# Kernel tuning notes

Hardware: AMD Instinct MI355X
Metric: run time of the kernel (lower is better)

## Reference

```python
import jax, jax.numpy as jnp
import numpy as np

B, L, E = 8, 2048, 128


def setup_inputs() -> dict:
    key = jax.random.key(0)
    k1, k2, k3, k4 = jax.random.split(key, 4)
    return {
        "Uq": jax.random.normal(k1, (B, L, E), dtype=jnp.float32),
        "Uid": jax.random.normal(k2, (B, L, E), dtype=jnp.float32),
        "mask": jnp.ones((L, L), dtype=jnp.float32),
        "Wc_w": jax.random.normal(k3, (3 * E,), dtype=jnp.float32) * 0.05,
        "Wc_b": jax.random.normal(k4, (), dtype=jnp.float32) * 0.05,
    }


def reference(Uq, Uid, mask, Wc_w, Wc_b):
    # Wc(cat(Uid, Uq, Uid*Uq)) decomposed into three direct projections —
    # exact same math as the Linear over the concatenation, never
    # materializing the [B, L, L, 3E] tensor.
    e = Uq.shape[-1]
    w_id, w_q, w_mul = Wc_w[:e], Wc_w[e:2 * e], Wc_w[2 * e:]
    s_id = jnp.einsum("bie,e->bi", Uid, w_id)          # [B, Lid]
    s_q = jnp.einsum("bje,e->bj", Uq, w_q)             # [B, Lq]
    s_mul = jnp.einsum("bie,bje,e->bij", Uid, Uq, w_mul)  # [B, Lid, Lq]
    S = (s_id[:, :, None] + s_q[:, None, :] + s_mul + Wc_b) * mask
    # S_D2Q = Softmax(dim=0) over the per-example [Lid, Lq] matrix -> axis=1
    P = jax.nn.softmax(S, axis=1)                      # [B, Lid, Lq]
    A_D2Q = jnp.einsum("bij,bje->bie", P, Uq)          # [B, Lid, E]
    M = jnp.einsum("bij,bkj->bik", P, P)               # P @ P^T, [B, Lid, Lid]
    A_Q2D = jnp.einsum("bik,bke->bie", M, Uid)         # [B, Lid, E]
    Vid = jnp.concatenate([Uid, A_D2Q, Uid * A_D2Q, Uid * A_Q2D], axis=-1)
    return Vid  # [B, Lid, 4E]
```

## Files before the change

### kernel.cpp

```cpp
#include <hip/hip_runtime.h>

#define L 2048
#define E 128
#define NB 8

typedef float f32x4 __attribute__((ext_vector_type(4)));
typedef short short8 __attribute__((ext_vector_type(8)));
typedef unsigned int u32;

static __device__ inline float bf2f(ushort u) {
  union { float f; u32 i; } v; v.i = ((u32)u) << 16; return v.f;
}
static __device__ inline ushort f2bf(float f) {
  union { float f; u32 i; } v; v.f = f;
  u32 x = v.i;
  return (ushort)((x + 0x7fffu + ((x >> 16) & 1u)) >> 16);
}

__device__ inline void glds16(const ushort* g, ushort* l) {
  __builtin_amdgcn_global_load_lds(
      (const __attribute__((address_space(1))) u32*)(const void*)g,
      (__attribute__((address_space(3))) u32*)(void*)l, 16, 0, 0);
}

__global__ __launch_bounds__(128) void k_prep(const float* __restrict__ Uq,
                                              const float* __restrict__ Uid,
                                              const float* __restrict__ Wcw,
                                              ushort* __restrict__ UqB,
                                              ushort* __restrict__ UidB,
                                              ushort* __restrict__ Uidw,
                                              float* __restrict__ s_id,
                                              float* __restrict__ s_q) {
  int r = blockIdx.x;
  int e = threadIdx.x;
  ushort uqu  = f2bf(Uq[(long)r * E + e]);
  ushort uidu = f2bf(Uid[(long)r * E + e]);
  float uqf = bf2f(uqu), uidf = bf2f(uidu);
  float wid  = bf2f(f2bf(Wcw[e]));
  float wq   = bf2f(f2bf(Wcw[E + e]));
  float wmul = bf2f(f2bf(Wcw[2 * E + e]));
  UqB[(long)r * E + e]  = uqu;
  UidB[(long)r * E + e] = uidu;
  Uidw[(long)r * E + e] = f2bf(uidf * wmul);
  float sid = uidf * wid, sq = uqf * wq;
  #pragma unroll
  for (int off = 32; off >= 1; off >>= 1) {
    sid += __shfl_down(sid, off, 64);
    sq  += __shfl_down(sq,  off, 64);
  }
  __shared__ float red[4];
  int wv = threadIdx.x >> 6;
  if ((threadIdx.x & 63) == 0) { red[wv * 2] = sid; red[wv * 2 + 1] = sq; }
  __syncthreads();
  if (threadIdx.x == 0) { s_id[r] = red[0] + red[2]; s_q[r] = red[1] + red[3]; }
}

__global__ __launch_bounds__(256) void k_maskT(const float* __restrict__ mask,
                                               ushort* __restrict__ maskT) {
  __shared__ ushort tile[32][33];
  int j0 = blockIdx.x * 32, i0 = blockIdx.y * 32;
  int tx = threadIdx.x, ty = threadIdx.y;
  #pragma unroll
  for (int r = ty; r < 32; r += 8)
    tile[r][tx] = f2bf(mask[(long)(i0 + r) * L + j0 + tx]);
  __syncthreads();
  #pragma unroll
  for (int r = ty; r < 32; r += 8)
    maskT[(long)(j0 + r) * L + i0 + tx] = tile[tx][r];
}

__global__ __launch_bounds__(256) void k_tr2(const ushort* __restrict__ s1,
                                             ushort* __restrict__ d1,
                                             const ushort* __restrict__ s2,
                                             ushort* __restrict__ d2) {
  __shared__ ushort tile[32][33];
  int zz = blockIdx.z;
  long base = (long)(zz & (NB - 1)) * L * E;
  const ushort* src = ((zz < NB) ? s1 : s2) + base;
  ushort* dst = ((zz < NB) ? d1 : d2) + base;
  int c0 = blockIdx.x * 32, r0 = blockIdx.y * 32;
  int tx = threadIdx.x, ty = threadIdx.y;
  #pragma unroll
  for (int i = ty; i < 32; i += 8)
    tile[i][tx] = src[(long)(r0 + i) * E + c0 + tx];
  __syncthreads();
  #pragma unroll
  for (int i = ty; i < 32; i += 8)
    dst[(long)(c0 + i) * L + r0 + tx] = tile[tx][i];
}

__device__ inline void gemm128_loop(const ushort* __restrict__ A,
                                    const ushort* __restrict__ B,
                                    long ldA, long ldB, int K,
                                    f32x4 acc[4][4],
                                    ushort* ldsA, ushort* ldsB) {
  const int t = threadIdx.x;
  const int w = t >> 6, lane = t & 63;
  const int mrow = lane & 15, quad = lane >> 4;
  const int lr = lane >> 3;
  const int lc = ((lane & 7) ^ lr) * 8;
  const int mh = (w & 1) * 64, nh = (w >> 1) * 64;
  for (int k0 = 0; k0 < K; k0 += 64) {
    __syncthreads();
    #pragma unroll
    for (int s = 0; s < 4; s++) {
      int row = w * 32 + s * 8 + lr;
      glds16(&A[(long)row * ldA + k0 + lc], &ldsA[w * 2048 + s * 512]);
      glds16(&B[(long)row * ldB + k0 + lc], &ldsB[w * 2048 + s * 512]);
    }
    __syncthreads();
    #pragma unroll
    for (int kk = 0; kk < 2; kk++) {
      short8 av[4], bv[4];
      #pragma unroll
      for (int mi = 0; mi < 4; mi++)
        av[mi] = *(const short8*)&ldsA[(mh + mi * 16 + mrow) * 64 +
                                       ((kk * 32 + quad * 8) ^ ((mrow & 7) << 3))];
      #pragma unroll
      for (int ni = 0; ni < 4; ni++)
        bv[ni] = *(const short8*)&ldsB[(nh + ni * 16 + mrow) * 64 +
                                       ((kk * 32 + quad * 8) ^ ((mrow & 7) << 3))];
      #pragma unroll
      for (int mi = 0; mi < 4; mi++)
        #pragma unroll
        for (int ni = 0; ni < 4; ni++)
          acc[mi][ni] = __builtin_amdgcn_mfma_f32_16x16x32_bf16(av[mi], bv[ni], acc[mi][ni], 0, 0, 0);
    }
  }
}

__device__ inline void gemm64x128_loop(const ushort* __restrict__ A,
                                       const ushort* __restrict__ B,
                                       long ldA, long ldB, int K,
                                       f32x4 acc[2][4],
                                       ushort* ldsA, ushort* ldsB) {
  const int t = threadIdx.x;
  const int w = t >> 6, lane = t & 63;
  const int mrow = lane & 15, quad = lane >> 4;
  const int lr = lane >> 3;
  const int lc = ((lane & 7) ^ lr) * 8;
  const int mh = (w & 1) * 32, nh = (w >> 1) * 64;
  for (int k0 = 0; k0 < K; k0 += 64) {
    __syncthreads();
    #pragma unroll
    for (int s = 0; s < 2; s++) {
      int row = w * 16 + s * 8 + lr;
      glds16(&A[(long)row * ldA + k0 + lc], &ldsA[w * 1024 + s * 512]);
    }
    #pragma unroll
    for (int s = 0; s < 4; s++) {
      int row = w * 32 + s * 8 + lr;
      glds16(&B[(long)row * ldB + k0 + lc], &ldsB[w * 2048 + s * 512]);
    }
    __syncthreads();
    #pragma unroll
    for (int kk = 0; kk < 2; kk++) {
      short8 av[2], bv[4];
      #pragma unroll
      for (int mi = 0; mi < 2; mi++)
        av[mi] = *(const short8*)&ldsA[(mh + mi * 16 + mrow) * 64 +
                                       ((kk * 32 + quad * 8) ^ ((mrow & 7) << 3))];
      #pragma unroll
      for (int ni = 0; ni < 4; ni++)
        bv[ni] = *(const short8*)&ldsB[(nh + ni * 16 + mrow) * 64 +
                                       ((kk * 32 + quad * 8) ^ ((mrow & 7) << 3))];
      #pragma unroll
      for (int mi = 0; mi < 2; mi++)
        #pragma unroll
        for (int ni = 0; ni < 4; ni++)
          acc[mi][ni] = __builtin_amdgcn_mfma_f32_16x16x32_bf16(av[mi], bv[ni], acc[mi][ni], 0, 0, 0);
    }
  }
}

__global__ __launch_bounds__(256) void k_scores(const ushort* __restrict__ Uq,
                                                const ushort* __restrict__ Uidw,
                                                const float* __restrict__ s_id,
                                                const float* __restrict__ s_q,
                                                const float* __restrict__ Wcb,
                                                const ushort* __restrict__ maskT,
                                                ushort* __restrict__ St,
                                                float* __restrict__ ps, int b0) {
  __shared__ ushort lds[16384];
  ushort* ldsA = lds;
  ushort* ldsB = lds + 8192;
  int bz = blockIdx.z, b = b0 + bz;
  int m0 = blockIdx.x * 128;
  int n0 = blockIdx.y * 128;
  int tile_i = blockIdx.y;
  const ushort* A = Uq   + (long)b * L * E + (long)m0 * E;
  const ushort* B = Uidw + (long)b * L * E + (long)n0 * E;
  f32x4 acc[4][4] = {};
  gemm128_loop(A, B, E, E, E, acc, ldsA, ldsB);
  float bias = bf2f(f2bf(Wcb[0]));
  const int t = threadIdx.x, w = t >> 6, lane = t & 63;
  const int col = lane & 15, quad = lane >> 4;
  const int mh = (w & 1) * 64, nh = (w >> 1) * 64;

  __syncthreads();
  float sidv[4];
  #pragma unroll
  for (int ni = 0; ni < 4; ni++)
    sidv[ni] = s_id[b * L + n0 + nh + ni * 16 + col];
  #pragma unroll
  for (int mi = 0; mi < 4; mi++) {
    float sqv[4];
    #pragma unroll
    for (int rg = 0; rg < 4; rg++)
      sqv[rg] = s_q[b * L + m0 + mh + mi * 16 + quad * 4 + rg];
    #pragma unroll
    for (int ni = 0; ni < 4; ni++) {
      int cl = nh + ni * 16 + col;
      #pragma unroll
      for (int rg = 0; rg < 4; rg++) {
        int row = mh + mi * 16 + quad * 4 + rg;
        float v = acc[mi][ni][rg] + sqv[rg] + sidv[ni] + bias;
        lds[row * 128 + (cl ^ ((row & 7) << 3))] = f2bf(v);
      }
    }
  }
  __syncthreads();
  #pragma unroll
  for (int p = 0; p < 8; p++) {
    int r2 = p * 16 + (t >> 4);
    int cu = (t & 15) * 8;
    uint4 sv = *(const uint4*)&lds[r2 * 128 + (cu ^ ((r2 & 7) << 3))];
    int jg = m0 + r2;
    uint4 mv = *(const uint4*)&maskT[(long)jg * L + n0 + cu];
    ushort o[8];
    float lsum = 0.f;
    const ushort* sp = (const ushort*)&sv;
    const ushort* mp = (const ushort*)&mv;
    #pragma unroll
    for (int k = 0; k < 8; k++) {
      float ev = __expf(bf2f(sp[k]) * bf2f(mp[k]));
      o[k] = f2bf(ev);
      lsum += bf2f(o[k]);
    }
    *(uint4*)&St[(long)bz * L * L + (long)jg * L + n0 + cu] = *(const uint4*)&o[0];
    #pragma unroll
    for (int off = 8; off >= 1; off >>= 1) lsum += __shfl_xor(lsum, off, 64);
    if ((t & 15) == 0) {
      ps[((long)bz * L + jg) * 16 + tile_i] = lsum;
    }
  }
}

__global__ __launch_bounds__(256) void k_redstats(const float* __restrict__ ps,
                                                  float* __restrict__ lg) {
  int idx = blockIdx.x * 256 + threadIdx.x;
  const float* psr = ps + (long)idx * 16;
  float s = 0.f;
  #pragma unroll
  for (int k = 0; k < 16; k++) s += psr[k];
  lg[idx] = 1.0f / s;
}

__global__ __launch_bounds__(256) void k_gemm_Tt(const ushort* __restrict__ UidT,
                                                 const ushort* __restrict__ Et,
                                                 const float* __restrict__ lg,
                                                 ushort* __restrict__ Tt, int b0) {
  __shared__ ushort lds[12288];
  ushort* ldsA = lds;
  ushort* ldsB = lds + 4096;
  int bz = blockIdx.z, b = b0 + bz;
  int e0 = (blockIdx.x & 1) * 64;
  int j0 = (blockIdx.x >> 1) * 128;
  const ushort* A = UidT + (long)b * E * L + (long)e0 * L;
  const ushort* B = Et   + (long)bz * L * L + (long)j0 * L;
  f32x4 acc[2][4] = {};
  gemm64x128_loop(A, B, L, L, L, acc, ldsA, ldsB);
  const int t = threadIdx.x, w = t >> 6, lane = t & 63;
  const int col = lane & 15, quad = lane >> 4;
  const int mh = (w & 1) * 32, nh = (w >> 1) * 64;
  __syncthreads();
  #pragma unroll
  for (int mi = 0; mi < 2; mi++)
    #pragma unroll
    for (int ni = 0; ni < 4; ni++) {
      int cl = nh + ni * 16 + col;
      float sc = lg[(long)bz * L + j0 + cl];
      #pragma unroll
      for (int rg = 0; rg < 4; rg++) {
        int row = mh + mi * 16 + quad * 4 + rg;
        lds[row * 128 + (cl ^ ((row & 7) << 3))] = f2bf(acc[mi][ni][rg] * sc);
      }
    }
  __syncthreads();
  #pragma unroll
  for (int p = 0; p < 4; p++) {
    int r2 = p * 16 + (t >> 4);
    int cu = (t & 15) * 8;
    uint4 v = *(const uint4*)&lds[r2 * 128 + (cu ^ ((r2 & 7) << 3))];
    *(uint4*)&Tt[(long)b * E * L + (long)(e0 + r2) * L + j0 + cu] = v;
  }
}

__global__ __launch_bounds__(256) void k_gemm_A(const ushort* __restrict__ Et,
                                                const ushort* __restrict__ UqT,
                                                const ushort* __restrict__ Tt,
                                                const ushort* __restrict__ UidB,
                                                const float* __restrict__ lg,
                                                float* __restrict__ out, int b0) {
  __shared__ ushort ldsA[64 * 72];
  __shared__ ushort ldsB[128 * 64];
  int bz = blockIdx.z, b = b0 + bz;
  int m0 = blockIdx.x * 64;
  int n0 = blockIdx.y * 128;
  const ushort* Eb = Et + (long)bz * L * L + m0;
  const float* lgb = lg + (long)bz * L;
  const ushort* B = (blockIdx.y == 0) ? (UqT + (long)b * E * L)
                                      : (Tt  + (long)b * E * L);
  const int t = threadIdx.x, w = t >> 6, lane = t & 63;
  const int mrow = lane & 15, quad = lane >> 4;
  const int lr = lane >> 3;
  const int lc = ((lane & 7) ^ lr) * 8;
  const int mh = (w & 1) * 32, nh = (w >> 1) * 64;
  const int jp2 = (t >> 3) * 2;
  const int ic  = (t & 7) * 8;
  f32x4 acc[2][4] = {};
  uint4 q0 = *(const uint4*)&Eb[(long)jp2 * L + ic];
  uint4 q1 = *(const uint4*)&Eb[(long)(jp2 + 1) * L + ic];
  float s0 = lgb[jp2], s1 = lgb[jp2 + 1];
  for (int k0 = 0; k0 < L; k0 += 64) {
    __syncthreads();
    #pragma unroll
    for (int s = 0; s < 4; s++) {
      int row = w * 32 + s * 8 + lr;
      glds16(&B[(long)row * L + k0 + lc], &ldsB[w * 2048 + s * 512]);
    }
    {
      const ushort* p0 = (const ushort*)&q0;
      const ushort* p1 = (const ushort*)&q1;
      #pragma unroll
      for (int k = 0; k < 8; k++) {
        u32 pk = (u32)f2bf(bf2f(p0[k]) * s0) |
                 ((u32)f2bf(bf2f(p1[k]) * s1) << 16);
        int i = ic + k;
        int cs = jp2 ^ (((i >> 3) & 7) << 3);
        *(u32*)&ldsA[i * 72 + cs] = pk;
      }
    }
    __syncthreads();
    if (k0 + 64 < L) {
      q0 = *(const uint4*)&Eb[(long)(k0 + 64 + jp2) * L + ic];
      q1 = *(const uint4*)&Eb[(long)(k0 + 64 + jp2 + 1) * L + ic];
      s0 = lgb[k0 + 64 + jp2]; s1 = lgb[k0 + 64 + jp2 + 1];
    }
    #pragma unroll
    for (int kk = 0; kk < 2; kk++) {
      short8 av[2], bv[4];
      #pragma unroll
      for (int mi = 0; mi < 2; mi++) {
        int i = mh + mi * 16 + mrow;
        av[mi] = *(const short8*)&ldsA[i * 72 +
                   ((kk * 32 + quad * 8) ^ (((i >> 3) & 7) << 3))];
      }
      #pragma unroll
      for (int ni = 0; ni < 4; ni++)
        bv[ni] = *(const short8*)&ldsB[(nh + ni * 16 + mrow) * 64 +
                                       ((kk * 32 + quad * 8) ^ ((mrow & 7) << 3))];
      #pragma unroll
      for (int mi = 0; mi < 2; mi++)
        #pragma unroll
        for (int ni = 0; ni < 4; ni++)
          acc[mi][ni] = __builtin_amdgcn_mfma_f32_16x16x32_bf16(av[mi], bv[ni], acc[mi][ni], 0, 0, 0);
    }
  }
  const int col = mrow;
  #pragma unroll
  for (int mi = 0; mi < 2; mi++)
    #pragma unroll
    for (int ni = 0; ni < 4; ni++)
      #pragma unroll
      for (int rg = 0; rg < 4; rg++) {
        int ig = m0 + mh + mi * 16 + quad * 4 + rg;
        int c  = n0 + nh + ni * 16 + col;
        float a = acc[mi][ni][rg];
        float uidf = bf2f(UidB[(long)b * L * E + (long)ig * E + (c & 127)]);
        long ob = ((long)b * L + ig) * 512;
        if (c < 128) {
          out[ob + c]       = uidf;
          out[ob + 128 + c] = a;
          out[ob + 256 + c] = uidf * a;
        } else {
          out[ob + 256 + c] = uidf * a;
        }
      }
}

extern "C" void kernel_launch(void* const* d_in, const int* in_sizes, int n_in,
                              void* d_out, int out_size, void* d_ws, size_t ws_size,
                              hipStream_t stream) {
  const float* Uq   = (const float*)d_in[0];
  const float* Uid  = (const float*)d_in[1];
  const float* mask = (const float*)d_in[2];
  const float* Wcw  = (const float*)d_in[3];
  const float* Wcb  = (const float*)d_in[4];
  float* out = (float*)d_out;

  char* ws = (char*)d_ws;
  size_t off = 0;
  auto alloc = [&](size_t bytes) -> void* {
    void* p = ws + off; off += (bytes + 255) & ~(size_t)255; return p;
  };
  const size_t nUb = (size_t)NB * L * E * 2;
  ushort* UqB   = (ushort*)alloc(nUb);
  ushort* UidB  = (ushort*)alloc(nUb);
  ushort* Uidw  = (ushort*)alloc(nUb);
  ushort* UqT   = (ushort*)alloc(nUb);
  ushort* UidT  = (ushort*)alloc(nUb);
  ushort* Tt    = (ushort*)alloc(nUb);
  ushort* maskT = (ushort*)alloc((size_t)L * L * 2);
  float*  s_id  = (float*)alloc((size_t)NB * L * 4);
  float*  s_q   = (float*)alloc((size_t)NB * L * 4);
  float*  lg    = (float*)alloc((size_t)NB * L * 4);
  float*  ps    = (float*)alloc((size_t)NB * L * 16 * 4);
  const size_t per_batch = (size_t)L * L * 2;
  size_t avail = (ws_size > off + per_batch) ? (ws_size - off) : per_batch;
  int nb_c = (int)(avail / per_batch);
  if (nb_c < 1) nb_c = 1;
  if (nb_c > NB) nb_c = NB;
  ushort* St = (ushort*)(ws + off);

  dim3 tb(32, 8);
  k_prep<<<NB * L, E, 0, stream>>>(Uq, Uid, Wcw, UqB, UidB, Uidw, s_id, s_q);
  k_maskT<<<dim3(L / 32, L / 32), tb, 0, stream>>>(mask, maskT);
  k_tr2<<<dim3(E / 32, L / 32, 2 * NB), tb, 0, stream>>>(UqB, UqT, UidB, UidT);

  for (int b0 = 0; b0 < NB; b0 += nb_c) {
    int nb = (NB - b0 < nb_c) ? (NB - b0) : nb_c;
    k_scores<<<dim3(L / 128, L / 128, nb), 256, 0, stream>>>(UqB, Uidw, s_id, s_q, Wcb, maskT, St, ps, b0);
    k_redstats<<<dim3(nb * L / 256), 256, 0, stream>>>(ps, lg);
    k_gemm_Tt<<<dim3(2 * (L / 128), 1, nb), 256, 0, stream>>>(UidT, St, lg, Tt, b0);
    k_gemm_A<<<dim3(L / 64, 2, nb), 256, 0, stream>>>(St, UqT, Tt, UidB, lg, out, b0);
  }
}
```

Before: 204.7 us.

## Double-buffer LDS tiles in Tt and A GEMM loops to overlap loads with MFMA

Replaces the single-buffered K loops in k_gemm_Tt and k_gemm_A with ping-pong LDS buffers. The next 64-wide K tile is issued via global_load_lds (and, for A, the scaled Et staging) before the MFMAs run on the current buffer. This drops one barrier per iteration and aims to hide global-to-LDS latency behind compute. In exchange it doubles LDS per block, to roughly 48–50 KB, which may lower occupancy.

```diff
diff --git a/kernel.cpp b/kernel.cpp
--- a/kernel.cpp
+++ b/kernel.cpp
@@ -129,7 +129,7 @@
   }
 }
 
-__device__ inline void gemm64x128_loop(const ushort* __restrict__ A,
+__device__ inline void gemm64x128_dbuf(const ushort* __restrict__ A,
                                        const ushort* __restrict__ B,
                                        long ldA, long ldB, int K,
                                        f32x4 acc[2][4],
@@ -140,36 +140,52 @@
   const int lr = lane >> 3;
   const int lc = ((lane & 7) ^ lr) * 8;
   const int mh = (w & 1) * 32, nh = (w >> 1) * 64;
+  #pragma unroll
+  for (int s = 0; s < 2; s++) {
+    int row = w * 16 + s * 8 + lr;
+    glds16(&A[(long)row * ldA + lc], &ldsA[w * 1024 + s * 512]);
+  }
+  #pragma unroll
+  for (int s = 0; s < 4; s++) {
+    int row = w * 32 + s * 8 + lr;
+    glds16(&B[(long)row * ldB + lc], &ldsB[w * 2048 + s * 512]);
+  }
+  int cur = 0;
   for (int k0 = 0; k0 < K; k0 += 64) {
     __syncthreads();
-    #pragma unroll
-    for (int s = 0; s < 2; s++) {
-      int row = w * 16 + s * 8 + lr;
-      glds16(&A[(long)row * ldA + k0 + lc], &ldsA[w * 1024 + s * 512]);
-    }
-    #pragma unroll
-    for (int s = 0; s < 4; s++) {
-      int row = w * 32 + s * 8 + lr;
-      glds16(&B[(long)row * ldB + k0 + lc], &ldsB[w * 2048 + s * 512]);
-    }
-    __syncthreads();
+    int nxt = cur ^ 1;
+    if (k0 + 64 < K) {
+      #pragma unroll
+      for (int s = 0; s < 2; s++) {
+        int row = w * 16 + s * 8 + lr;
+        glds16(&A[(long)row * ldA + k0 + 64 + lc], &ldsA[nxt * 4096 + w * 1024 + s * 512]);
+      }
+      #pragma unroll
+      for (int s = 0; s < 4; s++) {
+        int row = w * 32 + s * 8 + lr;
+        glds16(&B[(long)row * ldB + k0 + 64 + lc], &ldsB[nxt * 8192 + w * 2048 + s * 512]);
+      }
+    }
+    const ushort* cA = &ldsA[cur * 4096];
+    const ushort* cB = &ldsB[cur * 8192];
     #pragma unroll
     for (int kk = 0; kk < 2; kk++) {
       short8 av[2], bv[4];
       #pragma unroll
       for (int mi = 0; mi < 2; mi++)
-        av[mi] = *(const short8*)&ldsA[(mh + mi * 16 + mrow) * 64 +
-                                       ((kk * 32 + quad * 8) ^ ((mrow & 7) << 3))];
+        av[mi] = *(const short8*)&cA[(mh + mi * 16 + mrow) * 64 +
+                                     ((kk * 32 + quad * 8) ^ ((mrow & 7) << 3))];
       #pragma unroll
       for (int ni = 0; ni < 4; ni++)
-        bv[ni] = *(const short8*)&ldsB[(nh + ni * 16 + mrow) * 64 +
-                                       ((kk * 32 + quad * 8) ^ ((mrow & 7) << 3))];
+        bv[ni] = *(const short8*)&cB[(nh + ni * 16 + mrow) * 64 +
+                                     ((kk * 32 + quad * 8) ^ ((mrow & 7) << 3))];
       #pragma unroll
       for (int mi = 0; mi < 2; mi++)
         #pragma unroll
         for (int ni = 0; ni < 4; ni++)
           acc[mi][ni] = __builtin_amdgcn_mfma_f32_16x16x32_bf16(av[mi], bv[ni], acc[mi][ni], 0, 0, 0);
     }
+    cur = nxt;
   }
 }
 
@@ -260,16 +276,16 @@
                                                  const ushort* __restrict__ Et,
                                                  const float* __restrict__ lg,
                                                  ushort* __restrict__ Tt, int b0) {
-  __shared__ ushort lds[12288];
+  __shared__ ushort lds[24576];
   ushort* ldsA = lds;
-  ushort* ldsB = lds + 4096;
+  ushort* ldsB = lds + 8192;
   int bz = blockIdx.z, b = b0 + bz;
   int e0 = (blockIdx.x & 1) * 64;
   int j0 = (blockIdx.x >> 1) * 128;
   const ushort* A = UidT + (long)b * E * L + (long)e0 * L;
   const ushort* B = Et   + (long)bz * L * L + (long)j0 * L;
   f32x4 acc[2][4] = {};
-  gemm64x128_loop(A, B, L, L, L, acc, ldsA, ldsB);
+  gemm64x128_dbuf(A, B, L, L, L, acc, ldsA, ldsB);
   const int t = threadIdx.x, w = t >> 6, lane = t & 63;
   const int col = lane & 15, quad = lane >> 4;
   const int mh = (w & 1) * 32, nh = (w >> 1) * 64;
@@ -302,8 +318,8 @@
                                                 const ushort* __restrict__ UidB,
                                                 const float* __restrict__ lg,
                                                 float* __restrict__ out, int b0) {
-  __shared__ ushort ldsA[64 * 72];
-  __shared__ ushort ldsB[128 * 64];
+  __shared__ ushort ldsA[2 * 4608];
+  __shared__ ushort ldsB[2 * 8192];
   int bz = blockIdx.z, b = b0 + bz;
   int m0 = blockIdx.x * 64;
   int n0 = blockIdx.y * 128;
@@ -322,14 +338,37 @@
   uint4 q0 = *(const uint4*)&Eb[(long)jp2 * L + ic];
   uint4 q1 = *(const uint4*)&Eb[(long)(jp2 + 1) * L + ic];
   float s0 = lgb[jp2], s1 = lgb[jp2 + 1];
+  #pragma unroll
+  for (int s = 0; s < 4; s++) {
+    int row = w * 32 + s * 8 + lr;
+    glds16(&B[(long)row * L + lc], &ldsB[w * 2048 + s * 512]);
+  }
+  {
+    const ushort* p0 = (const ushort*)&q0;
+    const ushort* p1 = (const ushort*)&q1;
+    #pragma unroll
+    for (int k = 0; k < 8; k++) {
+      u32 pk = (u32)f2bf(bf2f(p0[k]) * s0) |
+               ((u32)f2bf(bf2f(p1[k]) * s1) << 16);
+      int i = ic + k;
+      int cs = jp2 ^ (((i >> 3) & 7) << 3);
+      *(u32*)&ldsA[i * 72 + cs] = pk;
+    }
+  }
+  q0 = *(const uint4*)&Eb[(long)(64 + jp2) * L + ic];
+  q1 = *(const uint4*)&Eb[(long)(64 + jp2 + 1) * L + ic];
+  s0 = lgb[64 + jp2]; s1 = lgb[64 + jp2 + 1];
+
+  int cur = 0;
   for (int k0 = 0; k0 < L; k0 += 64) {
     __syncthreads();
-    #pragma unroll
-    for (int s = 0; s < 4; s++) {
-      int row = w * 32 + s * 8 + lr;
-      glds16(&B[(long)row * L + k0 + lc], &ldsB[w * 2048 + s * 512]);
-    }
-    {
+    int nxt = cur ^ 1;
+    if (k0 + 64 < L) {
+      #pragma unroll
+      for (int s = 0; s < 4; s++) {
+        int row = w * 32 + s * 8 + lr;
+        glds16(&B[(long)row * L + k0 + 64 + lc], &ldsB[nxt * 8192 + w * 2048 + s * 512]);
+      }
       const ushort* p0 = (const ushort*)&q0;
       const ushort* p1 = (const ushort*)&q1;
       #pragma unroll
@@ -338,34 +377,36 @@
                  ((u32)f2bf(bf2f(p1[k]) * s1) << 16);
         int i = ic + k;
         int cs = jp2 ^ (((i >> 3) & 7) << 3);
-        *(u32*)&ldsA[i * 72 + cs] = pk;
-      }
-    }
-    __syncthreads();
-    if (k0 + 64 < L) {
-      q0 = *(const uint4*)&Eb[(long)(k0 + 64 + jp2) * L + ic];
-      q1 = *(const uint4*)&Eb[(long)(k0 + 64 + jp2 + 1) * L + ic];
-      s0 = lgb[k0 + 64 + jp2]; s1 = lgb[k0 + 64 + jp2 + 1];
-    }
+        *(u32*)&ldsA[nxt * 4608 + i * 72 + cs] = pk;
+      }
+    }
+    if (k0 + 128 < L) {
+      q0 = *(const uint4*)&Eb[(long)(k0 + 128 + jp2) * L + ic];
+      q1 = *(const uint4*)&Eb[(long)(k0 + 128 + jp2 + 1) * L + ic];
+      s0 = lgb[k0 + 128 + jp2]; s1 = lgb[k0 + 128 + jp2 + 1];
+    }
+    const ushort* cA = &ldsA[cur * 4608];
+    const ushort* cB = &ldsB[cur * 8192];
     #pragma unroll
     for (int kk = 0; kk < 2; kk++) {
       short8 av[2], bv[4];
       #pragma unroll
       for (int mi = 0; mi < 2; mi++) {
         int i = mh + mi * 16 + mrow;
-        av[mi] = *(const short8*)&ldsA[i * 72 +
+        av[mi] = *(const short8*)&cA[i * 72 +
                    ((kk * 32 + quad * 8) ^ (((i >> 3) & 7) << 3))];
       }
       #pragma unroll
       for (int ni = 0; ni < 4; ni++)
-        bv[ni] = *(const short8*)&ldsB[(nh + ni * 16 + mrow) * 64 +
-                                       ((kk * 32 + quad * 8) ^ ((mrow & 7) << 3))];
+        bv[ni] = *(const short8*)&cB[(nh + ni * 16 + mrow) * 64 +
+                                     ((kk * 32 + quad * 8) ^ ((mrow & 7) << 3))];
       #pragma unroll
       for (int mi = 0; mi < 2; mi++)
         #pragma unroll
         for (int ni = 0; ni < 4; ni++)
           acc[mi][ni] = __builtin_amdgcn_mfma_f32_16x16x32_bf16(av[mi], bv[ni], acc[mi][ni], 0, 0, 0);
     }
+    cur = nxt;
   }
   const int col = mrow;
   #pragma unroll
```

Result: no change. 205.7 us (+0.5%).
